# Kernel tuning notes

Hardware: AMD Instinct MI355X
Metric: run time of the kernel (lower is better)

Reference implementation:

```python
import jax, jax.numpy as jnp
import numpy as np

# module-level constants from the original repo
NUM_CLASSES = 4
CLASS_NONE = 0
RETINA_SIZE = 224.0

# loss weights (ContourLoss defaults)
POINT_W, ORIENT_W, CLASS_W, INTERSECT_W = 1.0, 0.5, 1.0, 0.1

B, S = 8, 2048


def setup_inputs() -> dict:
    key = jax.random.key(0)
    k1, k2, k3, k4, k5, k6, k7 = jax.random.split(key, 7)
    point_pred = jax.random.uniform(k1, (B, S, 2), jnp.float32) * RETINA_SIZE
    orient_pred = jax.random.normal(k2, (B, S, 2), jnp.float32)
    orient_pred = orient_pred / jnp.linalg.norm(orient_pred, axis=-1, keepdims=True)
    class_pred = jax.random.normal(k3, (B, S, NUM_CLASSES), jnp.float32)
    tgt_pts = jax.random.uniform(k4, (B, S, 2), jnp.float32) * RETINA_SIZE
    tgt_orient = jax.random.normal(k5, (B, S, 2), jnp.float32)
    tgt_orient = tgt_orient / jnp.linalg.norm(tgt_orient, axis=-1, keepdims=True)
    tgt_cls = jax.random.randint(k6, (B, S), 0, NUM_CLASSES).astype(jnp.float32)
    target_seq = jnp.concatenate([tgt_pts, tgt_orient, tgt_cls[..., None]], axis=-1)
    padding_mask = jax.random.bernoulli(k7, 0.15, (B, S))
    return {"point_pred": point_pred, "orient_pred": orient_pred,
            "class_pred": class_pred, "target_seq": target_seq,
            "padding_mask": padding_mask}


def _intersection_per_sample(pts, non_none):
    # pts: (S,2), non_none: (S,) bool.
    # Compact valid points to the front (stable), mirroring point_pred[b, valid_idx].
    order = jnp.argsort(jnp.logical_not(non_none), stable=True)
    pts_c = pts[order]                      # (S,2), first n rows valid
    n = non_none.sum()
    n_seg = n - 1
    starts, ends = pts_c[:-1], pts_c[1:]    # (S-1,2)
    M = S - 1
    ii = jnp.arange(M)[:, None]
    jj = jnp.arange(M)[None, :]
    mask = ((jj >= ii + 2) & (ii < n_seg) & (jj < n_seg)
            & ~((ii == 0) & (jj == n_seg - 1)) & (n >= 4))
    p1 = starts[:, None, :]; p2 = ends[:, None, :]   # segment i
    p3 = starts[None, :, :]; p4 = ends[None, :, :]   # segment j

    def cross(a, b, c):
        return ((b[..., 0] - a[..., 0]) * (c[..., 1] - a[..., 1])
                - (b[..., 1] - a[..., 1]) * (c[..., 0] - a[..., 0]))

    d1 = cross(p3, p4, p1)
    d2 = cross(p3, p4, p2)
    d3 = cross(p1, p2, p3)
    d4 = cross(p1, p2, p4)
    s = jax.nn.sigmoid(-d1 * d2 * 0.01) * jax.nn.sigmoid(-d3 * d4 * 0.01)
    return jnp.where(mask, s, 0.0).sum(), mask.sum()


def reference(point_pred, orient_pred, class_pred, target_seq, padding_mask):
    Bd, Sd, _ = class_pred.shape
    target_class = target_seq[:, :, 4].astype(jnp.int32)
    target_point = target_seq[:, :, :2]
    target_orient = target_seq[:, :, 2:4]
    valid = jnp.logical_not(padding_mask)
    valid_f = valid.astype(jnp.float32)

    # classification: cross entropy, masked mean over valid tokens
    logp = jax.nn.log_softmax(class_pred, axis=-1)
    cls = -jnp.take_along_axis(logp, target_class[..., None], axis=-1)[..., 0]
    cls_loss = (cls * valid_f).sum() / jnp.maximum(valid_f.sum(), 1.0)

    non_none = valid & (target_class != CLASS_NONE)
    nn_f = non_none.astype(jnp.float32)
    nn_denom = jnp.maximum(nn_f.sum(), 1.0)

    # point: SmoothL1 (beta=1) on normalized coords, mean over xy, masked mean
    d = (point_pred - target_point) / RETINA_SIZE
    ad = jnp.abs(d)
    sl1 = jnp.where(ad < 1.0, 0.5 * d * d, ad - 0.5).mean(axis=-1)
    pt_loss = (sl1 * nn_f).sum() / nn_denom

    # orientation: 1 - cosine similarity (orient_pred assumed L2-normalized)
    cos_sim = (orient_pred * target_orient).sum(axis=-1)
    orient_loss = ((1.0 - cos_sim) * nn_f).sum() / nn_denom

    # intersection penalty over non-adjacent segment pairs, per sample
    sums, counts = jax.vmap(_intersection_per_sample)(point_pred, non_none)
    cnt = counts.sum()
    intersect_loss = jnp.where(cnt > 0, sums.sum() / jnp.maximum(cnt, 1).astype(jnp.float32), 0.0)

    total = (POINT_W * pt_loss + ORIENT_W * orient_loss
             + CLASS_W * cls_loss + INTERSECT_W * intersect_loss)
    return (total, pt_loss, orient_loss, cls_loss, intersect_loss)
```

## Files before the change

kernel.cpp:

```cpp
#include <hip/hip_runtime.h>

#define B 8
#define S 2048
#define NBPS 128
#define NBLK_INTER (B * NBPS)
#define NBLK_LOSS 64
#define NBLK_TOTAL (NBLK_INTER + NBLK_LOSS)
#define TPB 256


__global__ __launch_bounds__(TPB) void mega_kernel(
    const float2* __restrict__ point_pred,
    const float2* __restrict__ orient_pred,
    const float4* __restrict__ class_pred,
    const float*  __restrict__ target_seq,
    const int*    __restrict__ padding_mask,
    int*   __restrict__ n_buf,
    float* __restrict__ partial,
    float* __restrict__ acc2)
{
    __shared__ float2 sp[S];
    __shared__ float red[TPB / 64][5];
    __shared__ int wsum[TPB / 64], woff[TPB / 64], nTot;

    const int blk = blockIdx.x;
    const int tid = threadIdx.x;
    const int lane = tid & 63, wv = tid >> 6;

    if (blk < NBLK_INTER) {
        const int b = blk >> 7;
        const int iblk = blk & (NBPS - 1);
        const int base = b * S;
        const int e0 = tid * 8;

        const int4* pm4 = (const int4*)(padding_mask + base + e0);
        const int4 ma = pm4[0], mb = pm4[1];
        const float4* tr4 = (const float4*)(target_seq + (size_t)(base + e0) * 5);
        float4 tq[10];
        #pragma unroll
        for (int k = 0; k < 10; ++k) tq[k] = tr4[k];
        float t4v[8];
        t4v[0] = tq[1].x; t4v[1] = tq[2].y; t4v[2] = tq[3].z; t4v[3] = tq[4].w;
        t4v[4] = tq[6].x; t4v[5] = tq[7].y; t4v[6] = tq[8].z; t4v[7] = tq[9].w;
        const float4* pq4 = (const float4*)(point_pred + base + e0);
        const float4 pa = pq4[0], pb = pq4[1], pc = pq4[2], pd = pq4[3];
        float2 p[8];
        p[0] = make_float2(pa.x, pa.y); p[1] = make_float2(pa.z, pa.w);
        p[2] = make_float2(pb.x, pb.y); p[3] = make_float2(pb.z, pb.w);
        p[4] = make_float2(pc.x, pc.y); p[5] = make_float2(pc.z, pc.w);
        p[6] = make_float2(pd.x, pd.y); p[7] = make_float2(pd.z, pd.w);
        int f[8];
        f[0] = (ma.x == 0 && (int)t4v[0] != 0) ? 1 : 0;
        f[1] = (ma.y == 0 && (int)t4v[1] != 0) ? 1 : 0;
        f[2] = (ma.z == 0 && (int)t4v[2] != 0) ? 1 : 0;
        f[3] = (ma.w == 0 && (int)t4v[3] != 0) ? 1 : 0;
        f[4] = (mb.x == 0 && (int)t4v[4] != 0) ? 1 : 0;
        f[5] = (mb.y == 0 && (int)t4v[5] != 0) ? 1 : 0;
        f[6] = (mb.z == 0 && (int)t4v[6] != 0) ? 1 : 0;
        f[7] = (mb.w == 0 && (int)t4v[7] != 0) ? 1 : 0;

        const int c = f[0]+f[1]+f[2]+f[3]+f[4]+f[5]+f[6]+f[7];
        int inc = c;
        #pragma unroll
        for (int off = 1; off < 64; off <<= 1) {
            int u = __shfl_up(inc, (unsigned)off, 64);
            if (lane >= off) inc += u;
        }
        if (lane == 63) wsum[wv] = inc;
        __syncthreads();
        if (tid == 0) {
            int run = 0;
            #pragma unroll
            for (int w = 0; w < TPB / 64; ++w) { woff[w] = run; run += wsum[w]; }
            nTot = run;
        }
        __syncthreads();
        int pos = woff[wv] + inc - c;
        #pragma unroll
        for (int k = 0; k < 8; ++k) { if (f[k]) sp[pos++] = p[k]; }
        __syncthreads();

        const int n = nTot;
        if (iblk == 0 && tid == 0) n_buf[b] = n;

        float local = 0.f;
        if (n >= 4) {
            const int n_seg = n - 1;
            for (int i = iblk; i < n_seg - 2; i += NBPS) {
                const float2 q1 = sp[i], q2 = sp[i + 1];
                const float e12x = q2.x - q1.x, e12y = q2.y - q1.y;
                const int jmax = (i == 0) ? n_seg - 1 : n_seg;
                for (int j = i + 2 + tid; j < jmax; j += TPB) {
                    const float2 q3 = sp[j], q4 = sp[j + 1];
                    const float e34x = q4.x - q3.x, e34y = q4.y - q3.y;
                    const float ce = e12x * e34y - e12y * e34x;
                    const float rx = q1.x - q3.x, ry = q1.y - q3.y;
                    const float d1 = e34x * ry - e34y * rx;
                    const float d3 = e12y * rx - e12x * ry;
                    const float d2 = d1 - ce;
                    const float d4 = d3 + ce;
                    const float ea = __expf(d1 * d2 * 0.01f);
                    const float eb = __expf(d3 * d4 * 0.01f);
                    local += __builtin_amdgcn_rcpf((1.f + ea) * (1.f + eb));
                }
            }
        }
        #pragma unroll
        for (int off = 32; off > 0; off >>= 1)
            local += __shfl_down(local, (unsigned)off, 64);
        if (lane == 0) red[wv][0] = local;
        __syncthreads();
        if (tid == 0)
            partial[blk] = red[0][0] + red[1][0] + red[2][0] + red[3][0];
    } else {
        const int idx = (blk - NBLK_INTER) * TPB + tid;
        const bool valid = (padding_mask[idx] == 0);
        const float t4 = target_seq[(size_t)idx * 5 + 4];
        const int tc = (int)t4;
        const bool nn = valid && (tc != 0);
        float cls_a = 0.f, pt_a = 0.f, or_a = 0.f, v_a = 0.f, nn_a = 0.f;
        if (valid) {
            const float4 cl = class_pred[idx];
            const float m = fmaxf(fmaxf(cl.x, cl.y), fmaxf(cl.z, cl.w));
            const float lse = m + logf(expf(cl.x - m) + expf(cl.y - m) +
                                       expf(cl.z - m) + expf(cl.w - m));
            const float ct = (tc == 0) ? cl.x : (tc == 1) ? cl.y : (tc == 2) ? cl.z : cl.w;
            cls_a = lse - ct;
            v_a = 1.f;
        }
        if (nn) {
            const float2 pp = point_pred[idx];
            const float tx = target_seq[(size_t)idx * 5 + 0];
            const float ty = target_seq[(size_t)idx * 5 + 1];
            const float dx = (pp.x - tx) * (1.0f / 224.0f);
            const float dy = (pp.y - ty) * (1.0f / 224.0f);
            const float adx = fabsf(dx), ady = fabsf(dy);
            const float l0 = (adx < 1.f) ? 0.5f * dx * dx : adx - 0.5f;
            const float l1 = (ady < 1.f) ? 0.5f * dy * dy : ady - 0.5f;
            pt_a = 0.5f * (l0 + l1);
            const float2 op = orient_pred[idx];
            const float ox = target_seq[(size_t)idx * 5 + 2];
            const float oy = target_seq[(size_t)idx * 5 + 3];
            or_a = 1.f - (op.x * ox + op.y * oy);
            nn_a = 1.f;
        }
        #pragma unroll
        for (int off = 32; off > 0; off >>= 1) {
            cls_a += __shfl_down(cls_a, (unsigned)off, 64);
            pt_a  += __shfl_down(pt_a,  (unsigned)off, 64);
            or_a  += __shfl_down(or_a,  (unsigned)off, 64);
            v_a   += __shfl_down(v_a,   (unsigned)off, 64);
            nn_a  += __shfl_down(nn_a,  (unsigned)off, 64);
        }
        if (lane == 0) {
            red[wv][0] = cls_a; red[wv][1] = pt_a; red[wv][2] = or_a;
            red[wv][3] = v_a;   red[wv][4] = nn_a;
        }
        __syncthreads();
        if (tid == 0) {
            const int lb = blk - NBLK_INTER;
            #pragma unroll
            for (int c5 = 0; c5 < 5; ++c5)
                acc2[c5 * NBLK_LOSS + lb] =
                    red[0][c5] + red[1][c5] + red[2][c5] + red[3][c5];
        }
    }
}

__global__ __launch_bounds__(64) void finalize_kernel(
    const float* __restrict__ acc2,
    const int* __restrict__ n_buf,
    const float* __restrict__ partial,
    float* __restrict__ out)
{
    const int lane = threadIdx.x;

    const float4* p4 = (const float4*)partial;
    float s = 0.f;
    #pragma unroll
    for (int k = 0; k < 4; ++k) {
        const float4 u = p4[lane * 4 + k];
        s += (u.x + u.y) + (u.z + u.w);
    }

    float a[5];
    #pragma unroll
    for (int ch = 0; ch < 5; ++ch) a[ch] = acc2[ch * NBLK_LOSS + lane];

    #pragma unroll
    for (int off = 32; off > 0; off >>= 1) {
        s += __shfl_down(s, (unsigned)off, 64);
        #pragma unroll
        for (int ch = 0; ch < 5; ++ch)
            a[ch] += __shfl_down(a[ch], (unsigned)off, 64);
    }

    if (lane == 0) {
        const float inter_sum = s;
        long long cnt = 0;
        #pragma unroll
        for (int b2 = 0; b2 < B; ++b2) {
            const int n = n_buf[b2];
            if (n >= 4) {
                const long long ns = n - 1;
                cnt += (ns - 1) * (ns - 2) / 2 - 1;
            }
        }
        const float cls_loss = a[0] / fmaxf(a[3], 1.f);
        const float pt_loss = a[1] / fmaxf(a[4], 1.f);
        const float orient_loss = a[2] / fmaxf(a[4], 1.f);
        const float intersect_loss = (cnt > 0) ? inter_sum / (float)cnt : 0.f;
        out[0] = 1.0f * pt_loss + 0.5f * orient_loss +
                 1.0f * cls_loss + 0.1f * intersect_loss;
        out[1] = pt_loss;
        out[2] = orient_loss;
        out[3] = cls_loss;
        out[4] = intersect_loss;
    }
}

extern "C" void kernel_launch(void* const* d_in, const int* in_sizes, int n_in,
                              void* d_out, int out_size, void* d_ws, size_t ws_size,
                              hipStream_t stream) {
    (void)in_sizes; (void)n_in; (void)out_size; (void)ws_size;
    const float2* point_pred  = (const float2*)d_in[0];
    const float2* orient_pred = (const float2*)d_in[1];
    const float4* class_pred  = (const float4*)d_in[2];
    const float*  target_seq  = (const float*)d_in[3];
    const int*    padding_mask = (const int*)d_in[4];

    int*   n_buf   = (int*)d_ws;
    float* partial = (float*)((char*)d_ws + 64);
    float* acc2    = (float*)((char*)d_ws + 4224);

    mega_kernel<<<NBLK_TOTAL, TPB, 0, stream>>>(point_pred, orient_pred,
                                                class_pred, target_seq,
                                                padding_mask,
                                                n_buf, partial, acc2);
    finalize_kernel<<<1, 64, 0, stream>>>(acc2, n_buf, partial, (float*)d_out);
}
```

Measured before the change: 19.76 us.

## Fuse finalize into mega kernel via spin-waited tagged slots

Removes the separate finalize kernel launch by adding one extra block that spin-waits on 64-bit slots tagged with a magic word, which the producer blocks write atomically. The extra block performs the final reduction and loss computation, then clears the slots for the next call. This saves a kernel launch and its gap, but it relies on the last block being scheduled, and on forward progress while the other blocks complete. It also adds global atomic polling traffic.

After: 21.76 us. 1.1x slower.

```diff
diff --git a/kernel.cpp b/kernel.cpp
--- a/kernel.cpp
+++ b/kernel.cpp
@@ -5,9 +5,27 @@
 #define NBPS 128
 #define NBLK_INTER (B * NBPS)
 #define NBLK_LOSS 64
-#define NBLK_TOTAL (NBLK_INTER + NBLK_LOSS)
+#define NBLK_TOTAL (NBLK_INTER + NBLK_LOSS + 1)
 #define TPB 256
-
+#define MAGIC 0xA5C97E31u
+
+typedef unsigned long long ull;
+typedef unsigned int uint;
+
+__device__ __forceinline__ void slot_store(ull* p, uint payload) {
+    __hip_atomic_store(p, ((ull)MAGIC << 32) | (ull)payload,
+                       __ATOMIC_RELAXED, __HIP_MEMORY_SCOPE_AGENT);
+}
+__device__ __forceinline__ uint slot_wait(ull* p) {
+    ull w;
+    do {
+        w = __hip_atomic_load(p, __ATOMIC_RELAXED, __HIP_MEMORY_SCOPE_AGENT);
+    } while ((uint)(w >> 32) != MAGIC);
+    return (uint)w;
+}
+__device__ __forceinline__ void slot_clear(ull* p) {
+    __hip_atomic_store(p, 0ull, __ATOMIC_RELAXED, __HIP_MEMORY_SCOPE_AGENT);
+}
 
 __global__ __launch_bounds__(TPB) void mega_kernel(
     const float2* __restrict__ point_pred,
@@ -15,13 +33,16 @@
     const float4* __restrict__ class_pred,
     const float*  __restrict__ target_seq,
     const int*    __restrict__ padding_mask,
-    int*   __restrict__ n_buf,
-    float* __restrict__ partial,
-    float* __restrict__ acc2)
+    ull* __restrict__ slots,
+    float* __restrict__ out)
 {
     __shared__ float2 sp[S];
     __shared__ float red[TPB / 64][5];
     __shared__ int wsum[TPB / 64], woff[TPB / 64], nTot;
+
+    ull* sp_partial = slots;
+    ull* sp_acc     = slots + NBLK_INTER;
+    ull* sp_nbuf    = slots + NBLK_INTER + 5 * NBLK_LOSS;
 
     const int blk = blockIdx.x;
     const int tid = threadIdx.x;
@@ -81,7 +102,7 @@
         __syncthreads();
 
         const int n = nTot;
-        if (iblk == 0 && tid == 0) n_buf[b] = n;
+        if (iblk == 0 && tid == 0) slot_store(&sp_nbuf[b], (uint)n);
 
         float local = 0.f;
         if (n >= 4) {
@@ -111,9 +132,11 @@
         if (lane == 0) red[wv][0] = local;
         __syncthreads();
         if (tid == 0)
-            partial[blk] = red[0][0] + red[1][0] + red[2][0] + red[3][0];
-    } else {
-        const int idx = (blk - NBLK_INTER) * TPB + tid;
+            slot_store(&sp_partial[blk],
+                       __float_as_uint(red[0][0] + red[1][0] + red[2][0] + red[3][0]));
+    } else if (blk < NBLK_INTER + NBLK_LOSS) {
+        const int lb = blk - NBLK_INTER;
+        const int idx = lb * TPB + tid;
         const bool valid = (padding_mask[idx] == 0);
         const float t4 = target_seq[(size_t)idx * 5 + 4];
         const int tc = (int)t4;
@@ -158,64 +181,69 @@
         }
         __syncthreads();
         if (tid == 0) {
-            const int lb = blk - NBLK_INTER;
             #pragma unroll
             for (int c5 = 0; c5 < 5; ++c5)
-                acc2[c5 * NBLK_LOSS + lb] =
-                    red[0][c5] + red[1][c5] + red[2][c5] + red[3][c5];
-        }
-    }
-}
-
-__global__ __launch_bounds__(64) void finalize_kernel(
-    const float* __restrict__ acc2,
-    const int* __restrict__ n_buf,
-    const float* __restrict__ partial,
-    float* __restrict__ out)
-{
-    const int lane = threadIdx.x;
-
-    const float4* p4 = (const float4*)partial;
-    float s = 0.f;
-    #pragma unroll
-    for (int k = 0; k < 4; ++k) {
-        const float4 u = p4[lane * 4 + k];
-        s += (u.x + u.y) + (u.z + u.w);
-    }
-
-    float a[5];
-    #pragma unroll
-    for (int ch = 0; ch < 5; ++ch) a[ch] = acc2[ch * NBLK_LOSS + lane];
-
-    #pragma unroll
-    for (int off = 32; off > 0; off >>= 1) {
-        s += __shfl_down(s, (unsigned)off, 64);
-        #pragma unroll
-        for (int ch = 0; ch < 5; ++ch)
-            a[ch] += __shfl_down(a[ch], (unsigned)off, 64);
-    }
-
-    if (lane == 0) {
-        const float inter_sum = s;
-        long long cnt = 0;
-        #pragma unroll
-        for (int b2 = 0; b2 < B; ++b2) {
-            const int n = n_buf[b2];
-            if (n >= 4) {
-                const long long ns = n - 1;
-                cnt += (ns - 1) * (ns - 2) / 2 - 1;
+                slot_store(&sp_acc[c5 * NBLK_LOSS + lb],
+                           __float_as_uint(red[0][c5] + red[1][c5] +
+                                           red[2][c5] + red[3][c5]));
+        }
+    } else {
+        float s = 0.f;
+        #pragma unroll
+        for (int k = 0; k < 4; ++k)
+            s += __uint_as_float(slot_wait(&sp_partial[tid + TPB * k]));
+        #pragma unroll
+        for (int off = 32; off > 0; off >>= 1)
+            s += __shfl_down(s, (unsigned)off, 64);
+        if (lane == 0) red[wv][0] = s;
+        __syncthreads();
+        const float inter_sum = red[0][0] + red[1][0] + red[2][0] + red[3][0];
+
+        float a[5] = {0.f, 0.f, 0.f, 0.f, 0.f};
+        if (wv == 0) {
+            #pragma unroll
+            for (int ch = 0; ch < 5; ++ch)
+                a[ch] = __uint_as_float(slot_wait(&sp_acc[ch * NBLK_LOSS + lane]));
+            #pragma unroll
+            for (int off = 32; off > 0; off >>= 1) {
+                #pragma unroll
+                for (int ch = 0; ch < 5; ++ch)
+                    a[ch] += __shfl_down(a[ch], (unsigned)off, 64);
             }
         }
-        const float cls_loss = a[0] / fmaxf(a[3], 1.f);
-        const float pt_loss = a[1] / fmaxf(a[4], 1.f);
-        const float orient_loss = a[2] / fmaxf(a[4], 1.f);
-        const float intersect_loss = (cnt > 0) ? inter_sum / (float)cnt : 0.f;
-        out[0] = 1.0f * pt_loss + 0.5f * orient_loss +
-                 1.0f * cls_loss + 0.1f * intersect_loss;
-        out[1] = pt_loss;
-        out[2] = orient_loss;
-        out[3] = cls_loss;
-        out[4] = intersect_loss;
+
+        if (tid == 0) {
+            long long cnt = 0;
+            #pragma unroll
+            for (int b2 = 0; b2 < B; ++b2) {
+                const int n = (int)slot_wait(&sp_nbuf[b2]);
+                if (n >= 4) {
+                    const long long ns = n - 1;
+                    cnt += (ns - 1) * (ns - 2) / 2 - 1;
+                }
+            }
+            const float cls_loss = a[0] / fmaxf(a[3], 1.f);
+            const float pt_loss = a[1] / fmaxf(a[4], 1.f);
+            const float orient_loss = a[2] / fmaxf(a[4], 1.f);
+            const float intersect_loss = (cnt > 0) ? inter_sum / (float)cnt : 0.f;
+            out[0] = 1.0f * pt_loss + 0.5f * orient_loss +
+                     1.0f * cls_loss + 0.1f * intersect_loss;
+            out[1] = pt_loss;
+            out[2] = orient_loss;
+            out[3] = cls_loss;
+            out[4] = intersect_loss;
+        }
+
+        #pragma unroll
+        for (int k = 0; k < 4; ++k) slot_clear(&sp_partial[tid + TPB * k]);
+        if (wv == 0) {
+            #pragma unroll
+            for (int ch = 0; ch < 5; ++ch) slot_clear(&sp_acc[ch * NBLK_LOSS + lane]);
+        }
+        if (tid == 0) {
+            #pragma unroll
+            for (int b2 = 0; b2 < B; ++b2) slot_clear(&sp_nbuf[b2]);
+        }
     }
 }
 
@@ -229,13 +257,8 @@
     const float*  target_seq  = (const float*)d_in[3];
     const int*    padding_mask = (const int*)d_in[4];
 
-    int*   n_buf   = (int*)d_ws;
-    float* partial = (float*)((char*)d_ws + 64);
-    float* acc2    = (float*)((char*)d_ws + 4224);
-
     mega_kernel<<<NBLK_TOTAL, TPB, 0, stream>>>(point_pred, orient_pred,
                                                 class_pred, target_seq,
                                                 padding_mask,
-                                                n_buf, partial, acc2);
-    finalize_kernel<<<1, 64, 0, stream>>>(acc2, n_buf, partial, (float*)d_out);
-}
+                                                (ull*)d_ws, (float*)d_out);
+}
```

## Split compaction into prep kernel and fuse finalize via packed atomic counter

Applied to the files above, without the earlier changes.

Moves per-sample stream compaction and the per-element losses into a small prep kernel that writes compacted points to workspace. The intersection kernel then loads the compacted points directly, and a spin-waiting last block finalizes the result. That block polls a single 64-bit atomic that packs a block count with a fixed-point sum, which removes the separate finalize launch and the 128-fold redundant compaction done per batch. The risks are a spin-wait that depends on all blocks being co-resident or scheduled before it, reduced fixed-point precision of the intersection sum, and an extra global round trip for the compacted points.

New measurement: 30.48 us. +54.2%, slower.

```diff
diff --git a/kernel.cpp b/kernel.cpp
--- a/kernel.cpp
+++ b/kernel.cpp
@@ -4,63 +4,46 @@
 #define S 2048
 #define NBPS 128
 #define NBLK_INTER (B * NBPS)
-#define NBLK_LOSS 64
-#define NBLK_TOTAL (NBLK_INTER + NBLK_LOSS)
 #define TPB 256
-
-
-__global__ __launch_bounds__(TPB) void mega_kernel(
+#define NLOSS_BLK 16
+#define FP_SCALE 16777216.0f
+#define CNT_SHIFT 48
+
+typedef unsigned long long ull;
+
+
+__global__ __launch_bounds__(1024) void prep_kernel(
+    const float4* __restrict__ point_pred4,
     const float2* __restrict__ point_pred,
     const float2* __restrict__ orient_pred,
     const float4* __restrict__ class_pred,
     const float*  __restrict__ target_seq,
     const int*    __restrict__ padding_mask,
+    ull*   __restrict__ fused_acc,
     int*   __restrict__ n_buf,
-    float* __restrict__ partial,
-    float* __restrict__ acc2)
+    float* __restrict__ acc2,
+    float2* __restrict__ pts_c)
 {
-    __shared__ float2 sp[S];
-    __shared__ float red[TPB / 64][5];
-    __shared__ int wsum[TPB / 64], woff[TPB / 64], nTot;
-
     const int blk = blockIdx.x;
     const int tid = threadIdx.x;
     const int lane = tid & 63, wv = tid >> 6;
 
-    if (blk < NBLK_INTER) {
-        const int b = blk >> 7;
-        const int iblk = blk & (NBPS - 1);
+    if (blk == 0 && tid == 0) *fused_acc = 0ull;
+
+    if (blk < B) {
+        const int b = blk;
         const int base = b * S;
-        const int e0 = tid * 8;
-
-        const int4* pm4 = (const int4*)(padding_mask + base + e0);
-        const int4 ma = pm4[0], mb = pm4[1];
-        const float4* tr4 = (const float4*)(target_seq + (size_t)(base + e0) * 5);
-        float4 tq[10];
-        #pragma unroll
-        for (int k = 0; k < 10; ++k) tq[k] = tr4[k];
-        float t4v[8];
-        t4v[0] = tq[1].x; t4v[1] = tq[2].y; t4v[2] = tq[3].z; t4v[3] = tq[4].w;
-        t4v[4] = tq[6].x; t4v[5] = tq[7].y; t4v[6] = tq[8].z; t4v[7] = tq[9].w;
-        const float4* pq4 = (const float4*)(point_pred + base + e0);
-        const float4 pa = pq4[0], pb = pq4[1], pc = pq4[2], pd = pq4[3];
-        float2 p[8];
-        p[0] = make_float2(pa.x, pa.y); p[1] = make_float2(pa.z, pa.w);
-        p[2] = make_float2(pb.x, pb.y); p[3] = make_float2(pb.z, pb.w);
-        p[4] = make_float2(pc.x, pc.y); p[5] = make_float2(pc.z, pc.w);
-        p[6] = make_float2(pd.x, pd.y); p[7] = make_float2(pd.z, pd.w);
-        int f[8];
-        f[0] = (ma.x == 0 && (int)t4v[0] != 0) ? 1 : 0;
-        f[1] = (ma.y == 0 && (int)t4v[1] != 0) ? 1 : 0;
-        f[2] = (ma.z == 0 && (int)t4v[2] != 0) ? 1 : 0;
-        f[3] = (ma.w == 0 && (int)t4v[3] != 0) ? 1 : 0;
-        f[4] = (mb.x == 0 && (int)t4v[4] != 0) ? 1 : 0;
-        f[5] = (mb.y == 0 && (int)t4v[5] != 0) ? 1 : 0;
-        f[6] = (mb.z == 0 && (int)t4v[6] != 0) ? 1 : 0;
-        f[7] = (mb.w == 0 && (int)t4v[7] != 0) ? 1 : 0;
-
-        const int c = f[0]+f[1]+f[2]+f[3]+f[4]+f[5]+f[6]+f[7];
-        int inc = c;
+        const int2* pm2 = (const int2*)(padding_mask + base);
+        const int2 mk = pm2[tid];
+        const float t4a = target_seq[(size_t)(base + tid * 2 + 0) * 5 + 4];
+        const float t4b = target_seq[(size_t)(base + tid * 2 + 1) * 5 + 4];
+        const float4 pp = point_pred4[(base >> 1) + tid];
+        const int f0 = (mk.x == 0 && (int)t4a != 0) ? 1 : 0;
+        const int f1 = (mk.y == 0 && (int)t4b != 0) ? 1 : 0;
+
+        __shared__ int wsum[16], woff[16];
+        const int tsum = f0 + f1;
+        int inc = tsum;
         #pragma unroll
         for (int off = 1; off < 64; off <<= 1) {
             int u = __shfl_up(inc, (unsigned)off, 64);
@@ -71,21 +54,99 @@
         if (tid == 0) {
             int run = 0;
             #pragma unroll
-            for (int w = 0; w < TPB / 64; ++w) { woff[w] = run; run += wsum[w]; }
-            nTot = run;
-        }
-        __syncthreads();
-        int pos = woff[wv] + inc - c;
-        #pragma unroll
-        for (int k = 0; k < 8; ++k) { if (f[k]) sp[pos++] = p[k]; }
-        __syncthreads();
-
-        const int n = nTot;
-        if (iblk == 0 && tid == 0) n_buf[b] = n;
-
+            for (int w = 0; w < 16; ++w) { woff[w] = run; run += wsum[w]; }
+            n_buf[b] = run;
+        }
+        __syncthreads();
+        const int pos = base + woff[wv] + (inc - tsum);
+        if (f0) pts_c[pos] = make_float2(pp.x, pp.y);
+        if (f1) pts_c[pos + f0] = make_float2(pp.z, pp.w);
+    } else {
+        const int lb = blk - B;
+        const int idx = lb * 1024 + tid;
+        const bool valid = (padding_mask[idx] == 0);
+        const float t4 = target_seq[(size_t)idx * 5 + 4];
+        const int tc = (int)t4;
+        const bool nn = valid && (tc != 0);
+        float cls_a = 0.f, pt_a = 0.f, or_a = 0.f, v_a = 0.f, nn_a = 0.f;
+        if (valid) {
+            const float4 cl = class_pred[idx];
+            const float m = fmaxf(fmaxf(cl.x, cl.y), fmaxf(cl.z, cl.w));
+            const float lse = m + logf(expf(cl.x - m) + expf(cl.y - m) +
+                                       expf(cl.z - m) + expf(cl.w - m));
+            const float ct = (tc == 0) ? cl.x : (tc == 1) ? cl.y : (tc == 2) ? cl.z : cl.w;
+            cls_a = lse - ct;
+            v_a = 1.f;
+        }
+        if (nn) {
+            const float2 pp = point_pred[idx];
+            const float tx = target_seq[(size_t)idx * 5 + 0];
+            const float ty = target_seq[(size_t)idx * 5 + 1];
+            const float dx = (pp.x - tx) * (1.0f / 224.0f);
+            const float dy = (pp.y - ty) * (1.0f / 224.0f);
+            const float adx = fabsf(dx), ady = fabsf(dy);
+            const float l0 = (adx < 1.f) ? 0.5f * dx * dx : adx - 0.5f;
+            const float l1 = (ady < 1.f) ? 0.5f * dy * dy : ady - 0.5f;
+            pt_a = 0.5f * (l0 + l1);
+            const float2 op = orient_pred[idx];
+            const float ox = target_seq[(size_t)idx * 5 + 2];
+            const float oy = target_seq[(size_t)idx * 5 + 3];
+            or_a = 1.f - (op.x * ox + op.y * oy);
+            nn_a = 1.f;
+        }
+        __shared__ float red[16][5];
+        #pragma unroll
+        for (int off = 32; off > 0; off >>= 1) {
+            cls_a += __shfl_down(cls_a, (unsigned)off, 64);
+            pt_a  += __shfl_down(pt_a,  (unsigned)off, 64);
+            or_a  += __shfl_down(or_a,  (unsigned)off, 64);
+            v_a   += __shfl_down(v_a,   (unsigned)off, 64);
+            nn_a  += __shfl_down(nn_a,  (unsigned)off, 64);
+        }
+        if (lane == 0) {
+            red[wv][0] = cls_a; red[wv][1] = pt_a; red[wv][2] = or_a;
+            red[wv][3] = v_a;   red[wv][4] = nn_a;
+        }
+        __syncthreads();
+        if (tid == 0) {
+            float s0 = 0, s1 = 0, s2 = 0, s3 = 0, s4 = 0;
+            #pragma unroll
+            for (int w = 0; w < 16; ++w) {
+                s0 += red[w][0]; s1 += red[w][1]; s2 += red[w][2];
+                s3 += red[w][3]; s4 += red[w][4];
+            }
+            acc2[0 * NLOSS_BLK + lb] = s0;
+            acc2[1 * NLOSS_BLK + lb] = s1;
+            acc2[2 * NLOSS_BLK + lb] = s2;
+            acc2[3 * NLOSS_BLK + lb] = s3;
+            acc2[4 * NLOSS_BLK + lb] = s4;
+        }
+    }
+}
+
+__global__ __launch_bounds__(TPB) void inter_kernel(
+    const float2* __restrict__ pts_c,
+    const int*   __restrict__ n_buf,
+    const float* __restrict__ acc2,
+    ull*   __restrict__ fused_acc,
+    float* __restrict__ out)
+{
+    const int blk = blockIdx.x;
+    const int tid = threadIdx.x;
+    const int lane = tid & 63, wv = tid >> 6;
+
+    if (blk < NBLK_INTER) {
+        __shared__ float2 sp[S];
+        __shared__ float red[TPB / 64];
+        const int b = blk >> 7;
+        const int iblk = blk & (NBPS - 1);
+        const int n = n_buf[b];
         float local = 0.f;
         if (n >= 4) {
             const int n_seg = n - 1;
+            const float2* pb = pts_c + b * S;
+            for (int k = tid; k < n; k += TPB) sp[k] = pb[k];
+            __syncthreads();
             for (int i = iblk; i < n_seg - 2; i += NBPS) {
                 const float2 q1 = sp[i], q2 = sp[i + 1];
                 const float e12x = q2.x - q1.x, e12y = q2.y - q1.y;
@@ -108,114 +169,58 @@
         #pragma unroll
         for (int off = 32; off > 0; off >>= 1)
             local += __shfl_down(local, (unsigned)off, 64);
-        if (lane == 0) red[wv][0] = local;
-        __syncthreads();
-        if (tid == 0)
-            partial[blk] = red[0][0] + red[1][0] + red[2][0] + red[3][0];
+        if (lane == 0) red[wv] = local;
+        __syncthreads();
+        if (tid == 0) {
+            const float bsum = red[0] + red[1] + red[2] + red[3];
+            const ull payload = ((ull)1 << CNT_SHIFT) + (ull)(bsum * FP_SCALE);
+            atomicAdd(fused_acc, payload);
+        }
     } else {
-        const int idx = (blk - NBLK_INTER) * TPB + tid;
-        const bool valid = (padding_mask[idx] == 0);
-        const float t4 = target_seq[(size_t)idx * 5 + 4];
-        const int tc = (int)t4;
-        const bool nn = valid && (tc != 0);
-        float cls_a = 0.f, pt_a = 0.f, or_a = 0.f, v_a = 0.f, nn_a = 0.f;
-        if (valid) {
-            const float4 cl = class_pred[idx];
-            const float m = fmaxf(fmaxf(cl.x, cl.y), fmaxf(cl.z, cl.w));
-            const float lse = m + logf(expf(cl.x - m) + expf(cl.y - m) +
-                                       expf(cl.z - m) + expf(cl.w - m));
-            const float ct = (tc == 0) ? cl.x : (tc == 1) ? cl.y : (tc == 2) ? cl.z : cl.w;
-            cls_a = lse - ct;
-            v_a = 1.f;
-        }
-        if (nn) {
-            const float2 pp = point_pred[idx];
-            const float tx = target_seq[(size_t)idx * 5 + 0];
-            const float ty = target_seq[(size_t)idx * 5 + 1];
-            const float dx = (pp.x - tx) * (1.0f / 224.0f);
-            const float dy = (pp.y - ty) * (1.0f / 224.0f);
-            const float adx = fabsf(dx), ady = fabsf(dy);
-            const float l0 = (adx < 1.f) ? 0.5f * dx * dx : adx - 0.5f;
-            const float l1 = (ady < 1.f) ? 0.5f * dy * dy : ady - 0.5f;
-            pt_a = 0.5f * (l0 + l1);
-            const float2 op = orient_pred[idx];
-            const float ox = target_seq[(size_t)idx * 5 + 2];
-            const float oy = target_seq[(size_t)idx * 5 + 3];
-            or_a = 1.f - (op.x * ox + op.y * oy);
-            nn_a = 1.f;
-        }
-        #pragma unroll
-        for (int off = 32; off > 0; off >>= 1) {
-            cls_a += __shfl_down(cls_a, (unsigned)off, 64);
-            pt_a  += __shfl_down(pt_a,  (unsigned)off, 64);
-            or_a  += __shfl_down(or_a,  (unsigned)off, 64);
-            v_a   += __shfl_down(v_a,   (unsigned)off, 64);
-            nn_a  += __shfl_down(nn_a,  (unsigned)off, 64);
-        }
+        if (wv != 0) return;
+        ull w;
+        do {
+            w = __hip_atomic_load(fused_acc, __ATOMIC_RELAXED,
+                                  __HIP_MEMORY_SCOPE_AGENT);
+        } while ((w >> CNT_SHIFT) != (ull)NBLK_INTER);
+        const float inter_sum =
+            (float)((double)(w & (((ull)1 << CNT_SHIFT) - 1)) *
+                    (1.0 / (double)FP_SCALE));
+
+        float a[5] = {0.f, 0.f, 0.f, 0.f, 0.f};
+        if (lane < NLOSS_BLK) {
+            #pragma unroll
+            for (int ch = 0; ch < 5; ++ch)
+                a[ch] = acc2[ch * NLOSS_BLK + lane];
+        }
+        #pragma unroll
+        for (int off = 8; off > 0; off >>= 1) {
+            #pragma unroll
+            for (int ch = 0; ch < 5; ++ch)
+                a[ch] += __shfl_down(a[ch], (unsigned)off, 64);
+        }
+
         if (lane == 0) {
-            red[wv][0] = cls_a; red[wv][1] = pt_a; red[wv][2] = or_a;
-            red[wv][3] = v_a;   red[wv][4] = nn_a;
-        }
-        __syncthreads();
-        if (tid == 0) {
-            const int lb = blk - NBLK_INTER;
-            #pragma unroll
-            for (int c5 = 0; c5 < 5; ++c5)
-                acc2[c5 * NBLK_LOSS + lb] =
-                    red[0][c5] + red[1][c5] + red[2][c5] + red[3][c5];
-        }
-    }
-}
-
-__global__ __launch_bounds__(64) void finalize_kernel(
-    const float* __restrict__ acc2,
-    const int* __restrict__ n_buf,
-    const float* __restrict__ partial,
-    float* __restrict__ out)
-{
-    const int lane = threadIdx.x;
-
-    const float4* p4 = (const float4*)partial;
-    float s = 0.f;
-    #pragma unroll
-    for (int k = 0; k < 4; ++k) {
-        const float4 u = p4[lane * 4 + k];
-        s += (u.x + u.y) + (u.z + u.w);
-    }
-
-    float a[5];
-    #pragma unroll
-    for (int ch = 0; ch < 5; ++ch) a[ch] = acc2[ch * NBLK_LOSS + lane];
-
-    #pragma unroll
-    for (int off = 32; off > 0; off >>= 1) {
-        s += __shfl_down(s, (unsigned)off, 64);
-        #pragma unroll
-        for (int ch = 0; ch < 5; ++ch)
-            a[ch] += __shfl_down(a[ch], (unsigned)off, 64);
-    }
-
-    if (lane == 0) {
-        const float inter_sum = s;
-        long long cnt = 0;
-        #pragma unroll
-        for (int b2 = 0; b2 < B; ++b2) {
-            const int n = n_buf[b2];
-            if (n >= 4) {
-                const long long ns = n - 1;
-                cnt += (ns - 1) * (ns - 2) / 2 - 1;
+            long long cnt = 0;
+            #pragma unroll
+            for (int b2 = 0; b2 < B; ++b2) {
+                const int n = n_buf[b2];
+                if (n >= 4) {
+                    const long long ns = n - 1;
+                    cnt += (ns - 1) * (ns - 2) / 2 - 1;
+                }
             }
-        }
-        const float cls_loss = a[0] / fmaxf(a[3], 1.f);
-        const float pt_loss = a[1] / fmaxf(a[4], 1.f);
-        const float orient_loss = a[2] / fmaxf(a[4], 1.f);
-        const float intersect_loss = (cnt > 0) ? inter_sum / (float)cnt : 0.f;
-        out[0] = 1.0f * pt_loss + 0.5f * orient_loss +
-                 1.0f * cls_loss + 0.1f * intersect_loss;
-        out[1] = pt_loss;
-        out[2] = orient_loss;
-        out[3] = cls_loss;
-        out[4] = intersect_loss;
+            const float cls_loss = a[0] / fmaxf(a[3], 1.f);
+            const float pt_loss = a[1] / fmaxf(a[4], 1.f);
+            const float orient_loss = a[2] / fmaxf(a[4], 1.f);
+            const float intersect_loss = (cnt > 0) ? inter_sum / (float)cnt : 0.f;
+            out[0] = 1.0f * pt_loss + 0.5f * orient_loss +
+                     1.0f * cls_loss + 0.1f * intersect_loss;
+            out[1] = pt_loss;
+            out[2] = orient_loss;
+            out[3] = cls_loss;
+            out[4] = intersect_loss;
+        }
     }
 }
 
@@ -229,13 +234,14 @@
     const float*  target_seq  = (const float*)d_in[3];
     const int*    padding_mask = (const int*)d_in[4];
 
-    int*   n_buf   = (int*)d_ws;
-    float* partial = (float*)((char*)d_ws + 64);
-    float* acc2    = (float*)((char*)d_ws + 4224);
-
-    mega_kernel<<<NBLK_TOTAL, TPB, 0, stream>>>(point_pred, orient_pred,
-                                                class_pred, target_seq,
-                                                padding_mask,
-                                                n_buf, partial, acc2);
-    finalize_kernel<<<1, 64, 0, stream>>>(acc2, n_buf, partial, (float*)d_out);
+    ull*    fused_acc = (ull*)d_ws;
+    int*    n_buf     = (int*)((char*)d_ws + 64);
+    float*  acc2      = (float*)((char*)d_ws + 128);
+    float2* pts_c     = (float2*)((char*)d_ws + 512);
+
+    prep_kernel<<<B + NLOSS_BLK, 1024, 0, stream>>>(
+        (const float4*)point_pred, point_pred, orient_pred, class_pred,
+        target_seq, padding_mask, fused_acc, n_buf, acc2, pts_c);
+    inter_kernel<<<NBLK_INTER + 1, TPB, 0, stream>>>(
+        pts_c, n_buf, acc2, fused_acc, (float*)d_out);
 }
```
